# Kernel optimization log

Hardware: AMD Instinct MI355X
Metric: run time of the kernel (lower is better)

The kernel has to match this reference:

```python
import jax, jax.numpy as jnp
import numpy as np

H = 32            # tsm_horizon
UNIT = H * 16     # block stride (512)
W = UNIT + H      # window size incl. h-step lookahead (544)
EPS = 1e-12

def setup_inputs() -> dict:
    key = jax.random.key(0)
    features = jax.random.normal(key, (8, 64, 8192), dtype=jnp.float32)
    return {"features": features}

def reference(features):
    # features: [B, C, L]  (post-TCN feature map); L divisible by UNIT
    B, C, L = features.shape
    nblocks = L // UNIT
    # pad L with H zeros so every block window has size W; corrcoef between two
    # time steps depends only on those two columns, so padded columns never
    # contaminate valid entries (they are masked out below).
    padded = jnp.pad(features, ((0, 0), (0, 0), (0, H)))
    starts = jnp.arange(nblocks) * UNIT                     # [n]
    idx = starts[:, None] + jnp.arange(W)[None, :]          # [n, W]
    windows = padded[:, :, idx]                             # [B, C, n, W]
    # corrcoef over channels: variables = time steps, observations = channels
    Xc = windows - windows.mean(axis=1, keepdims=True)      # center over C
    num = jnp.einsum('bcnw,bcnv->bnwv', Xc, Xc)             # [B, n, W, W]
    norm = jnp.sqrt(jnp.einsum('bcnw,bcnw->bnw', Xc, Xc))   # [B, n, W]
    corr = num / jnp.maximum(norm[..., :, None] * norm[..., None, :], EPS)
    # extract superdiagonal band: tsm[t, k] = corr[t, t+1+k], t<UNIT, k<H
    t = jnp.arange(UNIT)
    cols = t[:, None] + 1 + jnp.arange(H)[None, :]          # [UNIT, H]
    band = corr[:, :, t[:, None], cols]                     # [B, n, UNIT, H]
    # entries whose global column index falls beyond L are zero (torch pads 0)
    gcol = starts[:, None, None] + cols[None, :, :]         # [n, UNIT, H]
    band = jnp.where(gcol[None] < L, band, jnp.zeros((), band.dtype))
    tsm = band.reshape(B, L, H).transpose(0, 2, 1)          # [B, H, L]
    return tsm
```

## Files before the change

### kernel.cpp

```cpp
#include <hip/hip_runtime.h>
#include <math.h>

#define BB    8
#define CC    64
#define LL    8192
#define HH    32
#define UNITL 512
#define TC    256
#define WC    288
#define EPSF  1e-12f
#define BSTR  260

typedef __attribute__((ext_vector_type(8))) short bf16x8;
typedef __attribute__((ext_vector_type(4))) float f32x4;

union U {
    float xs[CC][WC];
    float band[HH][BSTR];
};

__global__ __launch_bounds__(512, 1)
void tsm_kernel(const float* __restrict__ feat, float* __restrict__ out) {
    __shared__ U u;
    __shared__ short xhi[WC * CC];
    __shared__ short xlo[WC * CC];
    __shared__ float ms[WC];
    __shared__ float ns[WC];

    const int tid  = threadIdx.x;
    const int lane = tid & 63;
    const int wv   = tid >> 6;
    const int blk  = blockIdx.x;
    const int half = blk & 1;
    const int n    = (blk >> 1) & 15;
    const int b    = blk >> 5;
    const int col0 = n * UNITL + half * TC;

    const float* fb = feat + (size_t)b * CC * LL;
    #pragma unroll
    for (int it = 0; it < 9; ++it) {
        int f16 = it * 512 + tid;
        int c   = f16 / 72;
        int q   = f16 - c * 72;
        int l   = col0 + 4 * q;
        f32x4 v = {0.f, 0.f, 0.f, 0.f};
        if (l < LL) v = *reinterpret_cast<const f32x4*>(fb + (size_t)c * LL + l);
        *reinterpret_cast<f32x4*>(&u.xs[c][4 * q]) = v;
    }
    __syncthreads();

    if (tid < WC) {
        int w = tid;
        float s = 0.f, ss = 0.f;
        #pragma unroll
        for (int c = 0; c < CC; ++c) { float x = u.xs[c][w]; s += x; ss += x * x; }
        float m = s * (1.0f / CC);
        ms[w] = m;
        ns[w] = sqrtf(fmaxf(ss - (float)CC * m * m, 0.f));
    }

    #pragma unroll
    for (int it = 0; it < 5; ++it) {
        int tau = it * 512 + tid;
        if (tau < WC * 8) {
            int c8 = tau / WC;
            int w  = tau - c8 * WC;
            bf16x8 Hv, Lv;
            #pragma unroll
            for (int j = 0; j < 8; ++j) {
                float x = u.xs[c8 * 8 + j][w];
                unsigned ub = __float_as_uint(x);
                unsigned hr = (ub + 0x7FFFu + ((ub >> 16) & 1u)) >> 16;
                float hf = __uint_as_float(hr << 16);
                float lo = x - hf;
                unsigned lb = __float_as_uint(lo);
                unsigned lr = (lb + 0x7FFFu + ((lb >> 16) & 1u)) >> 16;
                Hv[j] = (short)hr;
                Lv[j] = (short)lr;
            }
            int idx = (w * 64 + c8 * 8) ^ ((w & 7) << 3);
            *reinterpret_cast<bf16x8*>(&xhi[idx]) = Hv;
            *reinterpret_cast<bf16x8*>(&xlo[idx]) = Lv;
        }
    }
    __syncthreads();

    {
        const int r16 = lane & 15;
        const int g   = lane >> 4;
        bf16x8 fhi[4][2], flo[4][2];
        #pragma unroll
        for (int bb = 0; bb < 4; ++bb) {
            int row  = 16 * (2 * wv + bb) + r16;
            int base = row * 64;
            int sw   = (row & 7) << 3;
            #pragma unroll
            for (int kk = 0; kk < 2; ++kk) {
                int idx = (base + (g + 4 * kk) * 8) ^ sw;
                fhi[bb][kk] = *reinterpret_cast<const bf16x8*>(&xhi[idx]);
                flo[bb][kk] = *reinterpret_cast<const bf16x8*>(&xlo[idx]);
            }
        }
        #pragma unroll
        for (int ii = 0; ii < 2; ++ii) {
            const int i = 2 * wv + ii;
            #pragma unroll
            for (int dj = 0; dj < 3; ++dj) {
                const int jb = ii + dj;
                f32x4 acc = {0.f, 0.f, 0.f, 0.f};
                acc = __builtin_amdgcn_mfma_f32_16x16x32_bf16(fhi[ii][0], fhi[jb][0], acc, 0, 0, 0);
                acc = __builtin_amdgcn_mfma_f32_16x16x32_bf16(fhi[ii][1], fhi[jb][1], acc, 0, 0, 0);
                acc = __builtin_amdgcn_mfma_f32_16x16x32_bf16(fhi[ii][0], flo[jb][0], acc, 0, 0, 0);
                acc = __builtin_amdgcn_mfma_f32_16x16x32_bf16(fhi[ii][1], flo[jb][1], acc, 0, 0, 0);
                acc = __builtin_amdgcn_mfma_f32_16x16x32_bf16(flo[ii][0], fhi[jb][0], acc, 0, 0, 0);
                acc = __builtin_amdgcn_mfma_f32_16x16x32_bf16(flo[ii][1], fhi[jb][1], acc, 0, 0, 0);
                #pragma unroll
                for (int r = 0; r < 4; ++r) {
                    int t  = 16 * i + 4 * g + r;
                    int tp = 16 * (i + dj) + r16;
                    int h  = tp - t - 1;
                    if ((unsigned)h < 32u) u.band[h][t] = acc[r];
                }
            }
        }
    }
    __syncthreads();

    {
        const int h  = tid >> 4;
        const int cb = tid & 15;
        float* ob = out + ((size_t)b * HH + h) * LL + col0;
        #pragma unroll
        for (int k = 0; k < 4; ++k) {
            int c4 = cb + 16 * k;
            int t0 = 4 * c4;
            f32x4 v = *reinterpret_cast<const f32x4*>(&u.band[h][t0]);
            f32x4 res;
            #pragma unroll
            for (int e = 0; e < 4; ++e) {
                int t  = t0 + e;
                int tp = t + 1 + h;
                float num  = v[e] - (float)CC * ms[t] * ms[tp];
                float den  = fmaxf(ns[t] * ns[tp], EPSF);
                float corr = num * __builtin_amdgcn_rcpf(den);
                if (col0 + tp >= LL) corr = 0.f;
                res[e] = corr;
            }
            *reinterpret_cast<f32x4*>(ob + t0) = res;
        }
    }
}

extern "C" void kernel_launch(void* const* d_in, const int* in_sizes, int n_in,
                              void* d_out, int out_size, void* d_ws, size_t ws_size,
                              hipStream_t stream) {
    const float* feat = (const float*)d_in[0];
    float* out = (float*)d_out;
    tsm_kernel<<<dim3(256), dim3(512), 0, stream>>>(feat, out);
}
```

Before: 13.41 us.

## Split column tiles in four, stage bf16 hi/lo in two channel chunks to shrink LDS

Halves the per-block tile (128 columns plus a 32-column lookahead) and launches twice as many blocks. Each block stages the input in two 32-channel chunks, converting to packed bf16 hi/lo on load. Means and norms are then computed from the reconstructed hi+lo values instead of the fp32 originals. LDS drops enough to allow up to 4 blocks per CU, to raise occupancy and overlap. In exchange, the 32-column halo is now loaded redundantly by a larger share of blocks, extra barriers are added, and the statistics carry a small bf16 split error.

Result: no change. 13.53 us (+0.9%).

```diff
diff --git a/kernel.cpp b/kernel.cpp
--- a/kernel.cpp
+++ b/kernel.cpp
@@ -1,126 +1,144 @@
 #include <hip/hip_runtime.h>
 #include <math.h>
 
-#define BB    8
 #define CC    64
 #define LL    8192
 #define HH    32
 #define UNITL 512
-#define TC    256
-#define WC    288
+#define TC    128
+#define WC    160
+#define XSTR  72
+#define BSTR  132
 #define EPSF  1e-12f
-#define BSTR  260
 
 typedef __attribute__((ext_vector_type(8))) short bf16x8;
 typedef __attribute__((ext_vector_type(4))) float f32x4;
+typedef __attribute__((ext_vector_type(4))) unsigned int u32x4;
 
 union U {
-    float xs[CC][WC];
-    float band[HH][BSTR];
+    unsigned int xs[32][WC];
+    struct {
+        float band[HH][BSTR];
+        float ms[WC];
+        float ns[WC];
+    } s;
 };
 
-__global__ __launch_bounds__(512, 1)
+__device__ __forceinline__ unsigned rne_bf16(unsigned ub) {
+    return (ub + 0x7FFFu + ((ub >> 16) & 1u)) >> 16;
+}
+__device__ __forceinline__ float bf16_to_f(unsigned short h) {
+    return __uint_as_float(((unsigned)h) << 16);
+}
+
+__global__ __launch_bounds__(512, 4)
 void tsm_kernel(const float* __restrict__ feat, float* __restrict__ out) {
     __shared__ U u;
-    __shared__ short xhi[WC * CC];
-    __shared__ short xlo[WC * CC];
-    __shared__ float ms[WC];
-    __shared__ float ns[WC];
+    __shared__ short xhi[WC * XSTR];
+    __shared__ short xlo[WC * XSTR];
 
     const int tid  = threadIdx.x;
     const int lane = tid & 63;
     const int wv   = tid >> 6;
     const int blk  = blockIdx.x;
-    const int half = blk & 1;
-    const int n    = (blk >> 1) & 15;
-    const int b    = blk >> 5;
-    const int col0 = n * UNITL + half * TC;
+    const int q4   = blk & 3;
+    const int n    = (blk >> 2) & 15;
+    const int b    = blk >> 6;
+    const int col0 = n * UNITL + q4 * TC;
 
     const float* fb = feat + (size_t)b * CC * LL;
-    #pragma unroll
-    for (int it = 0; it < 9; ++it) {
-        int f16 = it * 512 + tid;
-        int c   = f16 / 72;
-        int q   = f16 - c * 72;
-        int l   = col0 + 4 * q;
-        f32x4 v = {0.f, 0.f, 0.f, 0.f};
-        if (l < LL) v = *reinterpret_cast<const f32x4*>(fb + (size_t)c * LL + l);
-        *reinterpret_cast<f32x4*>(&u.xs[c][4 * q]) = v;
+
+    for (int chunk = 0; chunk < 2; ++chunk) {
+        #pragma unroll
+        for (int it = 0; it < 3; ++it) {
+            int tau = it * 512 + tid;
+            if (tau < 32 * (WC / 4)) {
+                int c  = tau / (WC / 4);
+                int qq = tau - c * (WC / 4);
+                int l  = col0 + 4 * qq;
+                f32x4 v = {0.f, 0.f, 0.f, 0.f};
+                if (l < LL)
+                    v = *reinterpret_cast<const f32x4*>(fb + (size_t)(chunk * 32 + c) * LL + l);
+                u32x4 pk;
+                #pragma unroll
+                for (int e = 0; e < 4; ++e) {
+                    unsigned ub = __float_as_uint(v[e]);
+                    unsigned hr = rne_bf16(ub);
+                    float lo = v[e] - __uint_as_float(hr << 16);
+                    unsigned lr = rne_bf16(__float_as_uint(lo));
+                    pk[e] = (hr << 16) | (lr & 0xFFFFu);
+                }
+                *reinterpret_cast<u32x4*>(&u.xs[c][4 * qq]) = pk;
+            }
+        }
+        __syncthreads();
+        #pragma unroll
+        for (int it = 0; it < 2; ++it) {
+            int tau = it * 512 + tid;
+            if (tau < 4 * WC) {
+                int c8 = tau / WC;
+                int w  = tau - c8 * WC;
+                bf16x8 Hv, Lv;
+                #pragma unroll
+                for (int j = 0; j < 8; ++j) {
+                    unsigned p = u.xs[c8 * 8 + j][w];
+                    Hv[j] = (short)(p >> 16);
+                    Lv[j] = (short)(p & 0xFFFFu);
+                }
+                int base = w * XSTR + chunk * 32 + c8 * 8;
+                *reinterpret_cast<bf16x8*>(&xhi[base]) = Hv;
+                *reinterpret_cast<bf16x8*>(&xlo[base]) = Lv;
+            }
+        }
+        __syncthreads();
     }
-    __syncthreads();
 
     if (tid < WC) {
-        int w = tid;
         float s = 0.f, ss = 0.f;
         #pragma unroll
-        for (int c = 0; c < CC; ++c) { float x = u.xs[c][w]; s += x; ss += x * x; }
-        float m = s * (1.0f / CC);
-        ms[w] = m;
-        ns[w] = sqrtf(fmaxf(ss - (float)CC * m * m, 0.f));
-    }
-
-    #pragma unroll
-    for (int it = 0; it < 5; ++it) {
-        int tau = it * 512 + tid;
-        if (tau < WC * 8) {
-            int c8 = tau / WC;
-            int w  = tau - c8 * WC;
-            bf16x8 Hv, Lv;
+        for (int k = 0; k < 8; ++k) {
+            bf16x8 Hv = *reinterpret_cast<const bf16x8*>(&xhi[tid * XSTR + 8 * k]);
+            bf16x8 Lv = *reinterpret_cast<const bf16x8*>(&xlo[tid * XSTR + 8 * k]);
             #pragma unroll
             for (int j = 0; j < 8; ++j) {
-                float x = u.xs[c8 * 8 + j][w];
-                unsigned ub = __float_as_uint(x);
-                unsigned hr = (ub + 0x7FFFu + ((ub >> 16) & 1u)) >> 16;
-                float hf = __uint_as_float(hr << 16);
-                float lo = x - hf;
-                unsigned lb = __float_as_uint(lo);
-                unsigned lr = (lb + 0x7FFFu + ((lb >> 16) & 1u)) >> 16;
-                Hv[j] = (short)hr;
-                Lv[j] = (short)lr;
+                float x = bf16_to_f((unsigned short)Hv[j]) + bf16_to_f((unsigned short)Lv[j]);
+                s += x; ss += x * x;
             }
-            int idx = (w * 64 + c8 * 8) ^ ((w & 7) << 3);
-            *reinterpret_cast<bf16x8*>(&xhi[idx]) = Hv;
-            *reinterpret_cast<bf16x8*>(&xlo[idx]) = Lv;
         }
+        float m = s * (1.0f / CC);
+        u.s.ms[tid] = m;
+        u.s.ns[tid] = sqrtf(fmaxf(ss - (float)CC * m * m, 0.f));
     }
-    __syncthreads();
-
     {
         const int r16 = lane & 15;
         const int g   = lane >> 4;
-        bf16x8 fhi[4][2], flo[4][2];
+        bf16x8 fh[3][2], fl[3][2];
         #pragma unroll
-        for (int bb = 0; bb < 4; ++bb) {
-            int row  = 16 * (2 * wv + bb) + r16;
-            int base = row * 64;
-            int sw   = (row & 7) << 3;
+        for (int bb = 0; bb < 3; ++bb) {
+            int row  = 16 * (wv + bb) + r16;
+            int base = row * XSTR;
             #pragma unroll
             for (int kk = 0; kk < 2; ++kk) {
-                int idx = (base + (g + 4 * kk) * 8) ^ sw;
-                fhi[bb][kk] = *reinterpret_cast<const bf16x8*>(&xhi[idx]);
-                flo[bb][kk] = *reinterpret_cast<const bf16x8*>(&xlo[idx]);
+                int off = base + (g + 4 * kk) * 8;
+                fh[bb][kk] = *reinterpret_cast<const bf16x8*>(&xhi[off]);
+                fl[bb][kk] = *reinterpret_cast<const bf16x8*>(&xlo[off]);
             }
         }
         #pragma unroll
-        for (int ii = 0; ii < 2; ++ii) {
-            const int i = 2 * wv + ii;
+        for (int dj = 0; dj < 3; ++dj) {
+            f32x4 acc = {0.f, 0.f, 0.f, 0.f};
+            acc = __builtin_amdgcn_mfma_f32_16x16x32_bf16(fh[0][0], fh[dj][0], acc, 0, 0, 0);
+            acc = __builtin_amdgcn_mfma_f32_16x16x32_bf16(fh[0][1], fh[dj][1], acc, 0, 0, 0);
+            acc = __builtin_amdgcn_mfma_f32_16x16x32_bf16(fh[0][0], fl[dj][0], acc, 0, 0, 0);
+            acc = __builtin_amdgcn_mfma_f32_16x16x32_bf16(fh[0][1], fl[dj][1], acc, 0, 0, 0);
+            acc = __builtin_amdgcn_mfma_f32_16x16x32_bf16(fl[0][0], fh[dj][0], acc, 0, 0, 0);
+            acc = __builtin_amdgcn_mfma_f32_16x16x32_bf16(fl[0][1], fh[dj][1], acc, 0, 0, 0);
             #pragma unroll
-            for (int dj = 0; dj < 3; ++dj) {
-                const int jb = ii + dj;
-                f32x4 acc = {0.f, 0.f, 0.f, 0.f};
-                acc = __builtin_amdgcn_mfma_f32_16x16x32_bf16(fhi[ii][0], fhi[jb][0], acc, 0, 0, 0);
-                acc = __builtin_amdgcn_mfma_f32_16x16x32_bf16(fhi[ii][1], fhi[jb][1], acc, 0, 0, 0);
-                acc = __builtin_amdgcn_mfma_f32_16x16x32_bf16(fhi[ii][0], flo[jb][0], acc, 0, 0, 0);
-                acc = __builtin_amdgcn_mfma_f32_16x16x32_bf16(fhi[ii][1], flo[jb][1], acc, 0, 0, 0);
-                acc = __builtin_amdgcn_mfma_f32_16x16x32_bf16(flo[ii][0], fhi[jb][0], acc, 0, 0, 0);
-                acc = __builtin_amdgcn_mfma_f32_16x16x32_bf16(flo[ii][1], fhi[jb][1], acc, 0, 0, 0);
-                #pragma unroll
-                for (int r = 0; r < 4; ++r) {
-                    int t  = 16 * i + 4 * g + r;
-                    int tp = 16 * (i + dj) + r16;
-                    int h  = tp - t - 1;
-                    if ((unsigned)h < 32u) u.band[h][t] = acc[r];
-                }
+            for (int r = 0; r < 4; ++r) {
+                int t  = 16 * wv + 4 * g + r;
+                int tp = 16 * (wv + dj) + r16;
+                int h  = tp - t - 1;
+                if ((unsigned)h < 32u) u.s.band[h][t] = acc[r];
             }
         }
     }
@@ -131,17 +149,16 @@
         const int cb = tid & 15;
         float* ob = out + ((size_t)b * HH + h) * LL + col0;
         #pragma unroll
-        for (int k = 0; k < 4; ++k) {
-            int c4 = cb + 16 * k;
-            int t0 = 4 * c4;
-            f32x4 v = *reinterpret_cast<const f32x4*>(&u.band[h][t0]);
+        for (int k = 0; k < 2; ++k) {
+            int t0 = 4 * (cb + 16 * k);
+            f32x4 v = *reinterpret_cast<const f32x4*>(&u.s.band[h][t0]);
             f32x4 res;
             #pragma unroll
             for (int e = 0; e < 4; ++e) {
                 int t  = t0 + e;
                 int tp = t + 1 + h;
-                float num  = v[e] - (float)CC * ms[t] * ms[tp];
-                float den  = fmaxf(ns[t] * ns[tp], EPSF);
+                float num  = v[e] - (float)CC * u.s.ms[t] * u.s.ms[tp];
+                float den  = fmaxf(u.s.ns[t] * u.s.ns[tp], EPSF);
                 float corr = num * __builtin_amdgcn_rcpf(den);
                 if (col0 + tp >= LL) corr = 0.f;
                 res[e] = corr;
@@ -156,5 +173,5 @@
                               hipStream_t stream) {
     const float* feat = (const float*)d_in[0];
     float* out = (float*)d_out;
-    tsm_kernel<<<dim3(256), dim3(512), 0, stream>>>(feat, out);
+    tsm_kernel<<<dim3(512), dim3(512), 0, stream>>>(feat, out);
 }
```
